# Performance work log

Hardware: AMD Instinct MI355X
Metric: run time of the kernel (lower is better)

Reference implementation:

```python
import jax, jax.numpy as jnp
import numpy as np

NUM_QRYS = 300
NUM_CLASSES = 80
NUM_PAIRS = 4_000_000
NMS_CANDIDATES = 1000
NMS_THR = 0.65
MAX_SEGS = 100
REFINED_WEIGHT = 2.0
FH = FW = 256  # final mask grid resolution


def setup_inputs() -> dict:
    key = jax.random.key(0)
    k1, k2, k3, k4, k5, k6, k7 = jax.random.split(key, 7)
    cls_logits = jax.random.normal(k1, (NUM_QRYS, NUM_CLASSES + 1), jnp.float32)
    # valid xyxy boxes in normalized [0,1] coords
    b = jax.random.uniform(k2, (NUM_QRYS, 4), jnp.float32)
    x1 = b[:, 0] * 0.7
    y1 = b[:, 1] * 0.7
    x2 = x1 + 0.05 + b[:, 2] * 0.25
    y2 = y1 + 0.05 + b[:, 3] * 0.25
    pred_boxes = jnp.stack([x1, y1, x2, y2], axis=1)
    seg_logits = jax.random.normal(k3, (NUM_PAIRS,), jnp.float32)
    key_xy = jax.random.uniform(k4, (NUM_PAIRS, 2), jnp.float32)
    qry_ids = jax.random.randint(k5, (NUM_PAIRS,), 0, NUM_QRYS, jnp.int32)
    refined_mask = jax.random.randint(k6, (NUM_PAIRS,), 0, 2, jnp.int32).astype(bool)
    map_ids = jax.random.randint(k7, (NUM_PAIRS,), 0, 4, jnp.int32)
    return {"cls_logits": cls_logits, "pred_boxes": pred_boxes, "seg_logits": seg_logits,
            "key_xy": key_xy, "qry_ids": qry_ids, "refined_mask": refined_mask, "map_ids": map_ids}


def _box_iou(boxes):  # boxes: [C,4] xyxy -> [C,C]
    x1 = jnp.maximum(boxes[:, None, 0], boxes[None, :, 0])
    y1 = jnp.maximum(boxes[:, None, 1], boxes[None, :, 1])
    x2 = jnp.minimum(boxes[:, None, 2], boxes[None, :, 2])
    y2 = jnp.minimum(boxes[:, None, 3], boxes[None, :, 3])
    inter = jnp.clip(x2 - x1, 0.0) * jnp.clip(y2 - y1, 0.0)
    area = (boxes[:, 2] - boxes[:, 0]) * (boxes[:, 3] - boxes[:, 1])
    union = area[:, None] + area[None, :] - inter
    return inter / jnp.maximum(union, 1e-9)


def _nms_keep(iou, thr):
    # greedy NMS over score-sorted candidates (rows already in descending score order)
    C = iou.shape[0]
    idx = jnp.arange(C)
    def body(i, keep):
        sup = (iou[i] > thr) & (idx > i) & keep[i]
        return keep & ~sup
    return jax.lax.fori_loop(0, C, body, jnp.ones(C, dtype=bool))


def reference(cls_logits, pred_boxes, seg_logits, key_xy, qry_ids, refined_mask, map_ids):
    num_qrys = cls_logits.shape[0]
    # expand per-query class scores -> flat predictions (batch_size = 1)
    scores = jax.nn.sigmoid(cls_logits[:, :-1]).reshape(-1)          # [Q*C]
    feat_ids = jnp.repeat(jnp.arange(num_qrys), NUM_CLASSES)          # [Q*C]
    labels = jnp.tile(jnp.arange(NUM_CLASSES), num_qrys)              # [Q*C]
    # top-k candidates before NMS
    top_scores, cand = jax.lax.top_k(scores, NMS_CANDIDATES)
    cand_feats = feat_ids[cand]
    cand_labels = labels[cand]
    # class-aware (batched) NMS: offset boxes per label so classes don't suppress each other
    offs = cand_labels.astype(pred_boxes.dtype)[:, None] * 4.0
    cand_boxes = pred_boxes[cand_feats] + offs
    keep = _nms_keep(_box_iou(cand_boxes), NMS_THR)
    kept_scores = jnp.where(keep, top_scores, -jnp.inf)
    sel_scores, sel = jax.lax.top_k(kept_scores, MAX_SEGS)
    sel_scores = jnp.where(jnp.isfinite(sel_scores), sel_scores, 0.0)
    sel_feats = cand_feats[sel]
    # assemble per-query mask logit maps from sparse query-key pairs (scatter-max)
    px = jnp.clip((key_xy[:, 0] * FW).astype(jnp.int32), 0, FW - 1)
    py = jnp.clip((key_xy[:, 1] * FH).astype(jnp.int32), 0, FH - 1)
    w_logits = jnp.where(refined_mask, REFINED_WEIGHT * seg_logits, seg_logits)
    flat = qry_ids * (FH * FW) + py * FW + px                          # [num_pairs]
    qry_maps = jnp.full((num_qrys * FH * FW,), -1e4, cls_logits.dtype).at[flat].max(w_logits)
    qry_maps = qry_maps.reshape(num_qrys, FH, FW)
    mask_probs = jax.nn.sigmoid(qry_maps[sel_feats])                   # [MAX_SEGS, FH, FW]
    # score-weighted soft masks (float output; thresholding at mask_thr yields bool masks)
    return sel_scores[:, None, None] * mask_probs
```

## Files before the change

kernel.cpp:

```cpp
#include <hip/hip_runtime.h>

#define NQ        300
#define NC        80
#define NE        24000
#define CAND      1000
#define KSEL      100
#define NPAIRS    4000000
#define HB        4096
#define FHW       65536
#define NMS_THR_F 0.65f
#define MAPS_INIT 0x39E3BFFFu

__device__ __forceinline__ unsigned enc_f32(float f) {
    unsigned u = __float_as_uint(f);
    return (u & 0x80000000u) ? ~u : (u | 0x80000000u);
}
__device__ __forceinline__ float dec_f32(unsigned k) {
    unsigned u = (k & 0x80000000u) ? (k ^ 0x80000000u) : ~k;
    return __uint_as_float(u);
}

__global__ void k_init_maps(uint4* __restrict__ maps) {
    int i = blockIdx.x * 256 + threadIdx.x;
    uint4 v; v.x = v.y = v.z = v.w = MAPS_INIT;
    maps[i] = v;
}

__global__ __launch_bounds__(1024) void k_select_sort(
    const float* __restrict__ cls,
    const float* __restrict__ pboxes,
    float4* __restrict__ cboxes, float* __restrict__ cscore,
    int* __restrict__ cfeat, int* __restrict__ clabel)
{
    __shared__ unsigned long long sbuf[4096];
    unsigned* hist = (unsigned*)sbuf;
    __shared__ int sB, sCount, sN;
    int tid = threadIdx.x;

    for (int b = tid; b < HB; b += 1024) hist[b] = 0u;
    __syncthreads();

    unsigned long long lk[24];
    #pragma unroll
    for (int k = 0; k < 24; k++) {
        int e = tid + (k << 10);
        if (e < NE) {
            int q = e / NC, c = e - q * NC;
            float x = cls[q * (NC + 1) + c];
            float s = 1.f / (1.f + expf(-x));
            unsigned bits = __float_as_uint(s);
            lk[k] = ((unsigned long long)bits << 32) | (unsigned)(0xFFFFFFFFu - (unsigned)e);
            atomicAdd(&hist[bits >> 18], 1u);
        }
    }
    __syncthreads();

    if (tid == 0) {
        int acc = 0, B = 0;
        for (int b = HB - 1; b >= 0; b--) {
            acc += (int)hist[b];
            if (acc >= CAND) { B = b; break; }
        }
        sB = B; sCount = 0;
    }
    __syncthreads();
    unsigned B = (unsigned)sB;

    #pragma unroll
    for (int k = 0; k < 24; k++) {
        int e = tid + (k << 10);
        if (e < NE) {
            unsigned long long key = lk[k];
            if ((unsigned)(key >> 50) >= B) {
                int pos = atomicAdd(&sCount, 1);
                if (pos < 4096) sbuf[pos] = key;
            }
        }
    }
    __syncthreads();
    int n = min(sCount, 4096);
    int nsort = 1024; while (nsort < n) nsort <<= 1;
    for (int i = n + tid; i < nsort; i += 1024) sbuf[i] = 0ULL;
    __syncthreads();

    for (int k = 2; k <= nsort; k <<= 1) {
        for (int j = k >> 1; j > 0; j >>= 1) {
            for (int i = tid; i < nsort; i += 1024) {
                int ixj = i ^ j;
                if (ixj > i) {
                    unsigned long long a = sbuf[i], b = sbuf[ixj];
                    bool up = ((i & k) == 0);
                    if (up ? (a < b) : (a > b)) { sbuf[i] = b; sbuf[ixj] = a; }
                }
            }
            __syncthreads();
        }
    }

    if (tid < CAND) {
        unsigned long long key = sbuf[tid];
        unsigned bits = (unsigned)(key >> 32);
        unsigned e = 0xFFFFFFFFu - (unsigned)(key & 0xFFFFFFFFu);
        int feat = (int)e / NC, lab = (int)e - feat * NC;
        cscore[tid] = __uint_as_float(bits);
        cfeat[tid]  = feat;
        clabel[tid] = lab;
        float off = 4.f * (float)lab;
        float4 b;
        b.x = pboxes[feat * 4 + 0] + off; b.y = pboxes[feat * 4 + 1] + off;
        b.z = pboxes[feat * 4 + 2] + off; b.w = pboxes[feat * 4 + 3] + off;
        cboxes[tid] = b;
    }
}

__global__ __launch_bounds__(64) void k_nms(
    const float4* __restrict__ cboxes, const int* __restrict__ clabel,
    int* __restrict__ keepflag)
{
    int lab = blockIdx.x, lane = threadIdx.x;
    __shared__ int list[256];
    int base = 0;
    for (int c = 0; c < CAND; c += 64) {
        int i = c + lane;
        bool m = (i < CAND) && (clabel[i] == lab);
        unsigned long long bal = __ballot(m);
        int rank = __popcll(bal & ((1ULL << lane) - 1ULL));
        if (m && base + rank < 256) list[base + rank] = i;
        base += __popcll(bal);
    }
    __syncthreads();
    int n = min(base, 256);

    float4 bx[4]; float area[4];
    unsigned keepm = 0;
    #pragma unroll
    for (int s = 0; s < 4; s++) {
        int j = (s << 6) + lane;
        if (j < n) {
            bx[s] = cboxes[list[j]];
            area[s] = (bx[s].z - bx[s].x) * (bx[s].w - bx[s].y);
            keepm |= (1u << s);
        }
    }
    #pragma unroll
    for (int slot = 0; slot < 4; slot++) {
        int i0 = slot << 6;
        if (i0 >= n) break;
        int iend = min(64, n - i0);
        for (int l = 0; l < iend; l++) {
            int i = i0 + l;
            unsigned km = __shfl(keepm, l);
            bool keep_i = (km >> slot) & 1u;
            float bix = __shfl(bx[slot].x, l), biy = __shfl(bx[slot].y, l);
            float biz = __shfl(bx[slot].z, l), biw = __shfl(bx[slot].w, l);
            float ai  = __shfl(area[slot], l);
            if (keep_i) {
                #pragma unroll
                for (int s2 = 0; s2 < 4; s2++) {
                    int j = (s2 << 6) + lane;
                    if (j > i && j < n && ((keepm >> s2) & 1u)) {
                        float xx1 = fmaxf(bix, bx[s2].x), yy1 = fmaxf(biy, bx[s2].y);
                        float xx2 = fminf(biz, bx[s2].z), yy2 = fminf(biw, bx[s2].w);
                        float inter = fmaxf(xx2 - xx1, 0.f) * fmaxf(yy2 - yy1, 0.f);
                        float uni = ai + area[s2] - inter;
                        if (inter / fmaxf(uni, 1e-9f) > NMS_THR_F) keepm &= ~(1u << s2);
                    }
                }
            }
        }
    }
    #pragma unroll
    for (int s = 0; s < 4; s++) {
        int j = (s << 6) + lane;
        if (j < n) keepflag[list[j]] = (keepm >> s) & 1u;
    }
}

__global__ __launch_bounds__(64) void k_pick(
    const float* __restrict__ cscore, const int* __restrict__ cfeat,
    const int* __restrict__ keepflag,
    float* __restrict__ sel_score, int* __restrict__ sel_slot,
    int* __restrict__ qry2slot,
    const unsigned* __restrict__ refined_raw, unsigned* __restrict__ mode_flag)
{
    int lane = threadIdx.x;
    __shared__ float ss[KSEL];
    __shared__ int   sf[KSEL];
    __shared__ int   q2s[NQ];

    unsigned any = 0;
    for (int i = lane; i < 4096; i += 64) if (refined_raw[i] > 1u) any = 1;
    unsigned mode = (__ballot(any != 0) != 0ULL) ? 1u : 0u;

    int base = 0;
    for (int c = 0; c < CAND; c += 64) {
        int i = c + lane;
        bool k = (i < CAND) && (keepflag[i] != 0);
        unsigned long long bal = __ballot(k);
        int rank = __popcll(bal & ((1ULL << lane) - 1ULL));
        int pos = base + rank;
        if (k && pos < KSEL) { ss[pos] = cscore[i]; sf[pos] = cfeat[i]; }
        base += __popcll(bal);
    }
    for (int q = lane; q < NQ; q += 64) q2s[q] = -1;
    __syncthreads();
    if (lane == 0) {
        int nsel = min(base, KSEL), nslots = 0;
        for (int s = 0; s < KSEL; s++) {
            if (s < nsel) {
                int f = sf[s];
                int sl = q2s[f];
                if (sl < 0) { sl = nslots++; q2s[f] = sl; }
                sel_slot[s] = sl; sel_score[s] = ss[s];
            } else {
                sel_slot[s] = -1; sel_score[s] = 0.f;
            }
        }
        *mode_flag = mode;
    }
    __syncthreads();
    for (int q = lane; q < NQ; q += 64) qry2slot[q] = q2s[q];
}

__global__ void k_scatter(
    const float* __restrict__ seg, const float2* __restrict__ xy,
    const int* __restrict__ qry, const unsigned* __restrict__ refined_raw,
    const int* __restrict__ qry2slot, const unsigned* __restrict__ mode_flag,
    unsigned* __restrict__ maps)
{
    int i = blockIdx.x * 256 + threadIdx.x;
    int slot = qry2slot[qry[i]];
    if (slot < 0) return;
    float2 p = xy[i];
    int px = min(max((int)(p.x * 256.f), 0), 255);
    int py = min(max((int)(p.y * 256.f), 0), 255);
    float w = seg[i];
    bool ref;
    if (*mode_flag) ref = ((const unsigned char*)refined_raw)[i] != 0;
    else            ref = refined_raw[i] != 0;
    if (ref) w *= 2.f;
    atomicMax(&maps[slot * FHW + py * 256 + px], enc_f32(w));
}

__global__ void k_output(
    const unsigned* __restrict__ maps,
    const float* __restrict__ sel_score, const int* __restrict__ sel_slot,
    float* __restrict__ out)
{
    int i = blockIdx.x * 256 + threadIdx.x;
    int s = i >> 16;
    float sc = sel_score[s];
    int slot = sel_slot[s];
    float v = 0.f;
    if (slot >= 0) {
        float m = dec_f32(maps[slot * FHW + (i & 65535)]);
        v = sc / (1.f + expf(-m));
    }
    out[i] = v;
}

extern "C" void kernel_launch(void* const* d_in, const int* in_sizes, int n_in,
                              void* d_out, int out_size, void* d_ws, size_t ws_size,
                              hipStream_t stream) {
    const float*    cls     = (const float*)d_in[0];
    const float*    pboxes  = (const float*)d_in[1];
    const float*    seg     = (const float*)d_in[2];
    const float2*   xy      = (const float2*)d_in[3];
    const int*      qry     = (const int*)d_in[4];
    const unsigned* refined = (const unsigned*)d_in[5];
    float* out = (float*)d_out;

    char* ws = (char*)d_ws;
    unsigned*  maps      = (unsigned*)ws;
    float4*    cboxes    = (float4*)(ws + 26214400);
    float*     cscore    = (float*) (ws + 26230400);
    int*       cfeat     = (int*)   (ws + 26234400);
    int*       clabel    = (int*)   (ws + 26238400);
    int*       keepflag  = (int*)   (ws + 26242400);
    float*     sel_score = (float*) (ws + 26246400);
    int*       sel_slot  = (int*)   (ws + 26246800);
    int*       qry2slot  = (int*)   (ws + 26247200);
    unsigned*  mode_flag = (unsigned*)(ws + 26248400);

    k_init_maps  <<<6400, 256, 0, stream>>>((uint4*)maps);
    k_select_sort<<<1, 1024, 0, stream>>>(cls, pboxes, cboxes, cscore, cfeat, clabel);
    k_nms        <<<NC, 64, 0, stream>>>(cboxes, clabel, keepflag);
    k_pick       <<<1, 64, 0, stream>>>(cscore, cfeat, keepflag, sel_score, sel_slot,
                                        qry2slot, refined, mode_flag);
    k_scatter    <<<15625, 256, 0, stream>>>(seg, xy, qry, refined, qry2slot, mode_flag, maps);
    k_output     <<<25600, 256, 0, stream>>>(maps, sel_score, sel_slot, out);
}
```

Before: 277.0 us.

## Refine top-k threshold with subhistogram, register bitonic sort, vectorize scatter and output

The candidate selection adds a second-level 64-bin histogram inside the boundary bucket, which shrinks the candidate set so it usually fits a 1024-element bitonic sort. That sort keeps data in registers, using wavefront shuffles for small strides and LDS only for large ones. The scatter and output kernels now process four elements per thread with 128-bit loads and stores, cutting launch size and per-element overhead. Scatter warps whose four pairs all map to unselected queries exit early, and the fallback path keeps the older LDS sort for larger candidate counts.

```diff
diff --git a/kernel.cpp b/kernel.cpp
--- a/kernel.cpp
+++ b/kernel.cpp
@@ -34,10 +34,12 @@
 {
     __shared__ unsigned long long sbuf[4096];
     unsigned* hist = (unsigned*)sbuf;
-    __shared__ int sB, sCount, sN;
+    __shared__ unsigned subhist[64];
+    __shared__ int sB, sT, sAbove, sCount, sN;
     int tid = threadIdx.x;
 
     for (int b = tid; b < HB; b += 1024) hist[b] = 0u;
+    if (tid < 64) subhist[tid] = 0u;
     __syncthreads();
 
     unsigned long long lk[24];
@@ -61,39 +63,78 @@
             acc += (int)hist[b];
             if (acc >= CAND) { B = b; break; }
         }
-        sB = B; sCount = 0;
+        sB = B; sAbove = acc - (int)hist[B]; sCount = 0;
     }
     __syncthreads();
     unsigned B = (unsigned)sB;
+
+    #pragma unroll
+    for (int k = 0; k < 24; k++) {
+        int e = tid + (k << 10);
+        if (e < NE && (unsigned)(lk[k] >> 50) == B)
+            atomicAdd(&subhist[(unsigned)(lk[k] >> 44) & 63u], 1u);
+    }
+    __syncthreads();
+    if (tid == 0) {
+        int acc2 = sAbove, T = 0;
+        for (int t = 63; t >= 0; t--) {
+            acc2 += (int)subhist[t];
+            if (acc2 >= CAND) { T = t; break; }
+        }
+        sT = T; sN = acc2;
+    }
+    __syncthreads();
+    unsigned T = (unsigned)sT;
 
     #pragma unroll
     for (int k = 0; k < 24; k++) {
         int e = tid + (k << 10);
         if (e < NE) {
             unsigned long long key = lk[k];
-            if ((unsigned)(key >> 50) >= B) {
+            unsigned bkt = (unsigned)(key >> 50);
+            unsigned sub = (unsigned)(key >> 44) & 63u;
+            if (bkt > B || (bkt == B && sub >= T)) {
                 int pos = atomicAdd(&sCount, 1);
                 if (pos < 4096) sbuf[pos] = key;
             }
         }
     }
     __syncthreads();
-    int n = min(sCount, 4096);
-    int nsort = 1024; while (nsort < n) nsort <<= 1;
-    for (int i = n + tid; i < nsort; i += 1024) sbuf[i] = 0ULL;
-    __syncthreads();
-
-    for (int k = 2; k <= nsort; k <<= 1) {
-        for (int j = k >> 1; j > 0; j >>= 1) {
-            for (int i = tid; i < nsort; i += 1024) {
-                int ixj = i ^ j;
-                if (ixj > i) {
-                    unsigned long long a = sbuf[i], b = sbuf[ixj];
-                    bool up = ((i & k) == 0);
-                    if (up ? (a < b) : (a > b)) { sbuf[i] = b; sbuf[ixj] = a; }
+    int n = min(sN, 4096);
+
+    if (n <= 1024) {
+        unsigned long long r = (tid < n) ? sbuf[tid] : 0ULL;
+        for (int k = 2; k <= 1024; k <<= 1) {
+            for (int j = k >> 1; j > 0; j >>= 1) {
+                unsigned long long p;
+                if (j >= 64) {
+                    sbuf[tid] = r; __syncthreads();
+                    p = sbuf[tid ^ j]; __syncthreads();
+                } else {
+                    p = __shfl_xor(r, j, 64);
                 }
-            }
-            __syncthreads();
+                bool d = (tid & k) != 0, lower = (tid & j) == 0;
+                r = (d != lower) ? (r > p ? r : p) : (r < p ? r : p);
+            }
+        }
+        sbuf[tid] = r;
+        __syncthreads();
+    } else {
+        int nsort = 2048; while (nsort < n) nsort <<= 1;
+        for (int i = n + tid; i < nsort; i += 1024) sbuf[i] = 0ULL;
+        __syncthreads();
+        for (int k = 2; k <= nsort; k <<= 1) {
+            for (int j = k >> 1; j > 0; j >>= 1) {
+                for (int i = tid; i < nsort; i += 1024) {
+                    int ixj = i ^ j;
+                    if (ixj > i) {
+                        unsigned long long a = sbuf[i], b = sbuf[ixj];
+                        bool up = ((i & k) == 0);
+                        if (up ? (a < b) : (a > b)) { sbuf[i] = b; sbuf[ixj] = a; }
+                    }
+                }
+                __syncthreads();
+            }
         }
     }
 
@@ -222,41 +263,65 @@
     for (int q = lane; q < NQ; q += 64) qry2slot[q] = q2s[q];
 }
 
-__global__ void k_scatter(
+__global__ __launch_bounds__(256) void k_scatter(
     const float* __restrict__ seg, const float2* __restrict__ xy,
     const int* __restrict__ qry, const unsigned* __restrict__ refined_raw,
     const int* __restrict__ qry2slot, const unsigned* __restrict__ mode_flag,
     unsigned* __restrict__ maps)
 {
+    int t = blockIdx.x * 256 + threadIdx.x;
+    int base = t << 2;
+    if (base >= NPAIRS) return;
+
+    int4 q4 = ((const int4*)qry)[t];
+    int s0 = qry2slot[q4.x], s1 = qry2slot[q4.y];
+    int s2 = qry2slot[q4.z], s3 = qry2slot[q4.w];
+    if ((s0 & s1 & s2 & s3) < 0) return;
+
+    float4 sg   = ((const float4*)seg)[t];
+    float4 xy01 = ((const float4*)xy)[2 * t];
+    float4 xy23 = ((const float4*)xy)[2 * t + 1];
+    unsigned r0, r1, r2, r3;
+    if (*mode_flag) {
+        unsigned rb = refined_raw[t];
+        r0 = rb & 255u; r1 = (rb >> 8) & 255u; r2 = (rb >> 16) & 255u; r3 = rb >> 24;
+    } else {
+        uint4 rr = ((const uint4*)refined_raw)[t];
+        r0 = rr.x; r1 = rr.y; r2 = rr.z; r3 = rr.w;
+    }
+
+    #define DO_PAIR(S, PX, PY, W, R)                                              \
+        if (S >= 0) {                                                             \
+            int px = min(max((int)((PX) * 256.f), 0), 255);                       \
+            int py = min(max((int)((PY) * 256.f), 0), 255);                       \
+            float w = (R) ? 2.f * (W) : (W);                                      \
+            atomicMax(&maps[S * FHW + py * 256 + px], enc_f32(w));                \
+        }
+    DO_PAIR(s0, xy01.x, xy01.y, sg.x, r0)
+    DO_PAIR(s1, xy01.z, xy01.w, sg.y, r1)
+    DO_PAIR(s2, xy23.x, xy23.y, sg.z, r2)
+    DO_PAIR(s3, xy23.z, xy23.w, sg.w, r3)
+    #undef DO_PAIR
+}
+
+__global__ __launch_bounds__(256) void k_output(
+    const uint4* __restrict__ maps4,
+    const float* __restrict__ sel_score, const int* __restrict__ sel_slot,
+    float4* __restrict__ out4)
+{
     int i = blockIdx.x * 256 + threadIdx.x;
-    int slot = qry2slot[qry[i]];
-    if (slot < 0) return;
-    float2 p = xy[i];
-    int px = min(max((int)(p.x * 256.f), 0), 255);
-    int py = min(max((int)(p.y * 256.f), 0), 255);
-    float w = seg[i];
-    bool ref;
-    if (*mode_flag) ref = ((const unsigned char*)refined_raw)[i] != 0;
-    else            ref = refined_raw[i] != 0;
-    if (ref) w *= 2.f;
-    atomicMax(&maps[slot * FHW + py * 256 + px], enc_f32(w));
-}
-
-__global__ void k_output(
-    const unsigned* __restrict__ maps,
-    const float* __restrict__ sel_score, const int* __restrict__ sel_slot,
-    float* __restrict__ out)
-{
-    int i = blockIdx.x * 256 + threadIdx.x;
-    int s = i >> 16;
+    int s = i >> 14;
     float sc = sel_score[s];
     int slot = sel_slot[s];
-    float v = 0.f;
+    float4 v = {0.f, 0.f, 0.f, 0.f};
     if (slot >= 0) {
-        float m = dec_f32(maps[slot * FHW + (i & 65535)]);
-        v = sc / (1.f + expf(-m));
-    }
-    out[i] = v;
+        uint4 m = maps4[slot * (FHW / 4) + (i & 16383)];
+        v.x = sc / (1.f + expf(-dec_f32(m.x)));
+        v.y = sc / (1.f + expf(-dec_f32(m.y)));
+        v.z = sc / (1.f + expf(-dec_f32(m.z)));
+        v.w = sc / (1.f + expf(-dec_f32(m.w)));
+    }
+    out4[i] = v;
 }
 
 extern "C" void kernel_launch(void* const* d_in, const int* in_sizes, int n_in,
@@ -287,6 +352,7 @@
     k_nms        <<<NC, 64, 0, stream>>>(cboxes, clabel, keepflag);
     k_pick       <<<1, 64, 0, stream>>>(cscore, cfeat, keepflag, sel_score, sel_slot,
                                         qry2slot, refined, mode_flag);
-    k_scatter    <<<15625, 256, 0, stream>>>(seg, xy, qry, refined, qry2slot, mode_flag, maps);
-    k_output     <<<25600, 256, 0, stream>>>(maps, sel_score, sel_slot, out);
-}
+    k_scatter    <<<3907, 256, 0, stream>>>(seg, xy, qry, refined, qry2slot, mode_flag, maps);
+    k_output     <<<6400, 256, 0, stream>>>((const uint4*)maps, sel_score, sel_slot,
+                                            (float4*)out);
+}
```

After: 248.5 us. 1.11x faster.
